# Kernel tuning notes

Hardware: AMD Instinct MI355X
Metric: run time of the kernel (lower is better)

Reference implementation:

```python
import jax, jax.numpy as jnp
import numpy as np

H, D = 8, 16          # heads, head_dim
HID = H * D           # hidden_channels = 128
OUT = 64              # out_channels
N = 25_000            # nodes per node type (author, paper)
E = 250_000           # edges per relation
L = 2                 # num HGT layers
T = 2                 # node types
R = 2                 # edge types: (author->paper), (paper->author)
SCALE = 1.0 / np.sqrt(HID).astype(np.float32)


def setup_inputs() -> dict:
    key = jax.random.key(0)
    ks = jax.random.split(key, 16)
    f = lambda k, s: jax.random.normal(k, s, dtype=jnp.float32)
    return dict(
        x_author=f(ks[0], (N, HID)),
        x_paper=f(ks[1], (N, HID)),
        edge_writes=jax.random.randint(ks[2], (2, E), 0, N, dtype=jnp.int32),
        edge_rev=jax.random.randint(ks[3], (2, E), 0, N, dtype=jnp.int32),
        W_in=f(ks[4], (T, HID, HID)) * SCALE,
        b_in=jnp.zeros((T, HID), jnp.float32),
        Wq=f(ks[5], (L, T, HID, HID)) * SCALE,
        bq=jnp.zeros((L, T, HID), jnp.float32),
        Wk=f(ks[6], (L, T, HID, HID)) * SCALE,
        bk=jnp.zeros((L, T, HID), jnp.float32),
        Wv=f(ks[7], (L, T, HID, HID)) * SCALE,
        bv=jnp.zeros((L, T, HID), jnp.float32),
        Wa=f(ks[8], (L, T, HID, HID)) * SCALE,
        ba=jnp.zeros((L, T, HID), jnp.float32),
        skip=jnp.ones((L, T), jnp.float32),
        a_rel=f(ks[9], (L, R, H, D, D)) * (1.0 / np.sqrt(D).astype(np.float32)),
        m_rel=f(ks[10], (L, R, H, D, D)) * (1.0 / np.sqrt(D).astype(np.float32)),
        p_rel=jnp.ones((L, R, H), jnp.float32),
        W_out=f(ks[11], (HID, OUT)) * SCALE,
        b_out=jnp.zeros((OUT,), jnp.float32),
    )


def _seg_softmax(scores, seg, n):
    # scores [E, H]; softmax over edges sharing the same destination node.
    m = jax.ops.segment_max(scores, seg, num_segments=n)
    e = jnp.exp(scores - m[seg])
    s = jax.ops.segment_sum(e, seg, num_segments=n)
    return e / (s[seg] + 1e-16)


def _hnn_forward(x_author, x_paper, edge_writes, edge_rev, W_in, b_in, Wq, bq,
                 Wk, bk, Wv, bv, Wa, ba, skip, a_rel, m_rel, p_rel, W_out, b_out):
    # input projection per node type + relu
    xs = [jax.nn.relu(x_author @ W_in[0] + b_in[0]),
          jax.nn.relu(x_paper @ W_in[1] + b_in[1])]
    edges = [(0, 1, edge_writes), (1, 0, edge_rev)]  # (src_type, dst_type, edge_index)
    inv_sqrt_d = jnp.float32(1.0 / np.sqrt(D))
    for l in range(L):
        q = [(xs[t] @ Wq[l, t] + bq[l, t]).reshape(N, H, D) for t in range(T)]
        k = [(xs[t] @ Wk[l, t] + bk[l, t]).reshape(N, H, D) for t in range(T)]
        v = [(xs[t] @ Wv[l, t] + bv[l, t]).reshape(N, H, D) for t in range(T)]
        agg = [jnp.zeros((N, HID), xs[0].dtype) for _ in range(T)]
        for r, (s, t, ei) in enumerate(edges):
            src, dst = ei[0], ei[1]
            # per-relation transform of gathered keys/values: [E,H,D] x [H,D,D]
            k_e = jnp.einsum('ehd,hdf->ehf', k[s][src], a_rel[l, r])
            score = jnp.sum(q[t][dst] * k_e, axis=-1) * p_rel[l, r] * inv_sqrt_d  # [E,H]
            alpha = _seg_softmax(score, dst, N)
            v_e = jnp.einsum('ehd,hdf->ehf', v[s][src], m_rel[l, r])
            msg = (v_e * alpha[:, :, None]).reshape(E, HID)
            agg[t] = agg[t] + jax.ops.segment_sum(msg, dst, num_segments=N)
        new_xs = []
        for t in range(T):
            out = jax.nn.gelu(agg[t], approximate=False) @ Wa[l, t] + ba[l, t]
            beta = jax.nn.sigmoid(skip[l, t])
            new_xs.append(beta * out + (1.0 - beta) * xs[t])  # gated residual (in==out dims)
        xs = new_xs
    return (xs[0] @ W_out + b_out, xs[1] @ W_out + b_out)


def reference(x_author, x_paper, edge_writes, edge_rev, W_in, b_in, Wq, bq, Wk,
              bk, Wv, bv, Wa, ba, skip, a_rel, m_rel, p_rel, W_out, b_out):
    return _hnn_forward(x_author, x_paper, edge_writes, edge_rev, W_in, b_in,
                        Wq, bq, Wk, bk, Wv, bv, Wa, ba, skip, a_rel, m_rel,
                        p_rel, W_out, b_out)
```

## Files before the change

### kernel.cpp

```cpp
#include <hip/hip_runtime.h>
#include <math.h>

#define N_NODES 25000
#define E_EDGES 250000
#define HID 128
#define OUTC 64
#define NPB 98

using bf16x8 = __attribute__((ext_vector_type(8))) short;
using u16x8  = __attribute__((ext_vector_type(8))) unsigned short;
using f32x4  = __attribute__((ext_vector_type(4))) float;

__device__ __forceinline__ unsigned short f2bf(float f) {
    unsigned u = __float_as_uint(f);
    u = (u + 0x7fffu + ((u >> 16) & 1u)) >> 16;
    return (unsigned short)u;
}
__device__ __forceinline__ float bf2f(unsigned short h) {
    return __uint_as_float(((unsigned)h) << 16);
}
__device__ __forceinline__ float gelu_f(float x) {
    return 0.5f * x * (1.0f + erff(x * 0.70710678118654752440f));
}

__global__ void hist2(const int* __restrict__ e0, const int* __restrict__ e1,
                      int* __restrict__ cnt) {
    int r = blockIdx.y;
    const int* d = (r ? e1 : e0) + E_EDGES;
    int e = blockIdx.x * 256 + threadIdx.x;
    if (e < E_EDGES) atomicAdd(&cnt[r * N_NODES + d[e]], 1);
}

__global__ void csr_partial(const int* __restrict__ cnt, int* __restrict__ part) {
    int r = blockIdx.y, b = blockIdx.x, t = threadIdx.x;
    int idx = b * 256 + t;
    int v = (idx < N_NODES) ? cnt[r * N_NODES + idx] : 0;
    #pragma unroll
    for (int d = 1; d < 64; d <<= 1) v += __shfl_xor(v, d);
    __shared__ int ws[4];
    if ((t & 63) == 0) ws[t >> 6] = v;
    __syncthreads();
    if (t == 0) part[r * NPB + b] = ws[0] + ws[1] + ws[2] + ws[3];
}

__global__ void csr_scanpart(int* __restrict__ part) {
    int w = threadIdx.x >> 6, lane = threadIdx.x & 63;
    int base = w * NPB;
    int a = part[base + lane];
    int b = (lane < NPB - 64) ? part[base + 64 + lane] : 0;
    int va = a, vb = b;
    #pragma unroll
    for (int d = 1; d < 64; d <<= 1) { int u = __shfl_up(va, d); if (lane >= d) va += u; }
    #pragma unroll
    for (int d = 1; d < 64; d <<= 1) { int u = __shfl_up(vb, d); if (lane >= d) vb += u; }
    int tot0 = __shfl(va, 63);
    part[base + lane] = va - a;
    if (lane < NPB - 64) part[base + 64 + lane] = vb - b + tot0;
}

__global__ void csr_write(int* __restrict__ cnt, const int* __restrict__ part,
                          int* __restrict__ rowptr) {
    int r = blockIdx.y, b = blockIdx.x, t = threadIdx.x;
    int idx = b * 256 + t;
    int v = (idx < N_NODES) ? cnt[r * N_NODES + idx] : 0;
    int lane = t & 63, w = t >> 6;
    int iv = v;
    #pragma unroll
    for (int d = 1; d < 64; d <<= 1) { int u = __shfl_up(iv, d); if (lane >= d) iv += u; }
    __shared__ int wtot[4];
    if (lane == 63) wtot[w] = iv;
    __syncthreads();
    int woff = part[r * NPB + b];
    #pragma unroll
    for (int i = 0; i < 4; i++) if (i < w) woff += wtot[i];
    int excl = woff + iv - v;
    if (idx < N_NODES) {
        rowptr[r * (N_NODES + 1) + idx] = excl;
        cnt[r * N_NODES + idx] = excl;
    }
    if (b == 0 && t == 0) rowptr[r * (N_NODES + 1) + N_NODES] = E_EDGES;
}

__global__ void scatter2(const int* __restrict__ e0, const int* __restrict__ e1,
                         int* __restrict__ cursor, int* __restrict__ srcs) {
    int r = blockIdx.y;
    const int* e = r ? e1 : e0;
    int i = blockIdx.x * 256 + threadIdx.x;
    if (i < E_EDGES) {
        int p = atomicAdd(&cursor[r * N_NODES + e[E_EDGES + i]], 1);
        srcs[r * E_EDGES + p] = e[i];
    }
}

__global__ void tconv(const float* __restrict__ src, unsigned short* __restrict__ dst, int C) {
    int m = blockIdx.y;
    int idx = blockIdx.x * 256 + threadIdx.x;
    if (idx >= C * 128) return;
    int c = idx >> 7, k = idx & 127;
    dst[(size_t)m * C * 128 + idx] = f2bf(src[(size_t)m * 128 * C + k * C + c]);
}

__global__ __launch_bounds__(256) void prep_qkv(
    const float* __restrict__ Wq, const float* __restrict__ bq,
    const float* __restrict__ Wk, const float* __restrict__ bk,
    const float* __restrict__ Wv, const float* __restrict__ bv,
    const float* __restrict__ a_rel, const float* __restrict__ m_rel,
    unsigned short* __restrict__ WT, float* __restrict__ bfq)
{
    int p = blockIdx.y;
    __shared__ float sA[2048], sM[2048];
    for (int i = threadIdx.x; i < 2048; i += 256) {
        sA[i] = a_rel[p * 2048 + i];
        sM[i] = m_rel[p * 2048 + i];
    }
    __syncthreads();
    int idx = blockIdx.x * 256 + threadIdx.x;
    if (idx >= 384 * 129) return;
    int c = idx / 129;
    int ik = idx - c * 129;
    const float* wq = Wq + (size_t)p * 16384;
    const float* wk = Wk + (size_t)p * 16384;
    const float* wv = Wv + (size_t)p * 16384;
    float val;
    if (c < 128) {
        val = (ik < 128) ? wq[ik * 128 + c] : bq[p * 128 + c];
    } else if (c < 256) {
        int cc = c - 128, h = cc >> 4, f = cc & 15;
        const float* row = (ik < 128) ? &wk[ik * 128 + h * 16] : &bk[p * 128 + h * 16];
        float s = 0.f;
        #pragma unroll
        for (int d = 0; d < 16; d++) s = fmaf(row[d], sA[h * 256 + d * 16 + f], s);
        val = s;
    } else {
        int cc = c - 256, h = cc >> 4, f = cc & 15;
        const float* row = (ik < 128) ? &wv[ik * 128 + h * 16] : &bv[p * 128 + h * 16];
        float s = 0.f;
        #pragma unroll
        for (int d = 0; d < 16; d++) s = fmaf(row[d], sM[h * 256 + d * 16 + f], s);
        val = s;
    }
    if (ik < 128) WT[(size_t)p * 384 * 128 + (size_t)c * 128 + ik] = f2bf(val);
    else bfq[p * 384 + c] = val;
}

template<int NOUT, int BN, int OUTMODE, int A_FP32, int KVIL>
__global__ __launch_bounds__(256) void mm4_kernel(
    const void* __restrict__ A0, const void* __restrict__ A1,
    const unsigned short* __restrict__ W0, const unsigned short* __restrict__ W1,
    const float* __restrict__ b0, const float* __restrict__ b1,
    const unsigned short* __restrict__ res0, const unsigned short* __restrict__ res1,
    const float* __restrict__ skipp,
    void* __restrict__ C0, void* __restrict__ C1, int nrows)
{
    constexpr int CF = BN / 16;
    __shared__ unsigned short sW[BN * 128];
    int z = blockIdx.z;
    const void* Av = z ? A1 : A0;
    const unsigned short* W = z ? W1 : W0;
    const float* bias = z ? b1 : b0;
    const unsigned short* res = z ? res1 : res0;
    void* Cv = z ? C1 : C0;

    int t = threadIdx.x;
    int w = t >> 6, lane = t & 63, lo = lane & 15, hi = lane >> 4;
    int col0 = blockIdx.y * BN;
    int rowbase = blockIdx.x * 128 + w * 32;

    const unsigned short* Wg = W + (size_t)col0 * 128;
    #pragma unroll
    for (int it = 0; it < BN / 16; ++it) {
        int idx = it * 256 + t;
        int col = idx >> 4, ch = idx & 15;
        bf16x8 v = *(const bf16x8*)(Wg + (size_t)col * 128 + ch * 8);
        *(bf16x8*)&sW[col * 128 + ((ch ^ (col & 7)) << 3)] = v;
    }

    bf16x8 a[2][4];
    #pragma unroll
    for (int rf = 0; rf < 2; rf++) {
        int r = rowbase + rf * 16 + lo;
        if (r > nrows - 1) r = nrows - 1;
        if (A_FP32) {
            const float* Arow = (const float*)Av + (size_t)r * HID;
            #pragma unroll
            for (int kk = 0; kk < 4; kk++) {
                float4 x0 = *(const float4*)(Arow + kk * 32 + hi * 8);
                float4 x1 = *(const float4*)(Arow + kk * 32 + hi * 8 + 4);
                bf16x8 v;
                v[0] = (short)f2bf(x0.x); v[1] = (short)f2bf(x0.y);
                v[2] = (short)f2bf(x0.z); v[3] = (short)f2bf(x0.w);
                v[4] = (short)f2bf(x1.x); v[5] = (short)f2bf(x1.y);
                v[6] = (short)f2bf(x1.z); v[7] = (short)f2bf(x1.w);
                a[rf][kk] = v;
            }
        } else {
            const unsigned short* Arow = (const unsigned short*)Av + (size_t)r * HID;
            #pragma unroll
            for (int kk = 0; kk < 4; kk++)
                a[rf][kk] = *(const bf16x8*)(Arow + kk * 32 + hi * 8);
        }
    }
    __syncthreads();

    f32x4 acc[2][CF];
    #pragma unroll
    for (int rf = 0; rf < 2; rf++)
        #pragma unroll
        for (int cf = 0; cf < CF; cf++) acc[rf][cf] = (f32x4){0.f, 0.f, 0.f, 0.f};

    #pragma unroll
    for (int cf = 0; cf < CF; cf++) {
        int colb = cf * 16 + lo;
        int sbase = colb * 128;
        int sx = colb & 7;
        bf16x8 bfr[4];
        #pragma unroll
        for (int kk = 0; kk < 4; kk++) {
            int ch = kk * 4 + hi;
            bfr[kk] = *(const bf16x8*)&sW[sbase + ((ch ^ sx) << 3)];
        }
        #pragma unroll
        for (int kk = 0; kk < 4; kk++) {
            acc[0][cf] = __builtin_amdgcn_mfma_f32_16x16x32_bf16(a[0][kk], bfr[kk], acc[0][cf], 0, 0, 0);
            acc[1][cf] = __builtin_amdgcn_mfma_f32_16x16x32_bf16(a[1][kk], bfr[kk], acc[1][cf], 0, 0, 0);
        }
    }

    float beta = 0.f, omb = 0.f;
    if (OUTMODE == 2) { float sv = skipp[z]; beta = 1.f / (1.f + __expf(-sv)); omb = 1.f - beta; }
    #pragma unroll
    for (int rf = 0; rf < 2; rf++) {
        #pragma unroll
        for (int cf = 0; cf < CF; cf++) {
            int col = col0 + cf * 16 + lo;
            float bb = bias[col];
            int scol = col;
            if (KVIL) {
                if (col >= 256)      { int cc = col - 256; scol = 128 + ((cc >> 2) << 3) + 4 + (cc & 3); }
                else if (col >= 128) { int cc = col - 128; scol = 128 + ((cc >> 2) << 3) + (cc & 3); }
            }
            #pragma unroll
            for (int j = 0; j < 4; j++) {
                int r = rowbase + rf * 16 + hi * 4 + j;
                if (r >= nrows) continue;
                float v = acc[rf][cf][j] + bb;
                if (OUTMODE == 1) v = fmaxf(v, 0.f);
                if (OUTMODE == 2) v = beta * v + omb * bf2f(res[(size_t)r * NOUT + col]);
                if (OUTMODE == 3) ((float*)Cv)[(size_t)r * NOUT + col] = v;
                else ((unsigned short*)Cv)[(size_t)r * NOUT + scol] = f2bf(v);
            }
        }
    }
}

__global__ __launch_bounds__(256) void attn5_kernel(
    const unsigned short* __restrict__ qkv0, const unsigned short* __restrict__ qkv1,
    const int* __restrict__ rowptr, const int* __restrict__ srcs,
    const float* __restrict__ prel,
    unsigned short* __restrict__ agg0, unsigned short* __restrict__ agg1, int n)
{
    int r = blockIdx.y;
    const unsigned short* qd = r ? qkv0 : qkv1;
    const unsigned short* sv = r ? qkv1 : qkv0;
    unsigned short* agg      = r ? agg0 : agg1;
    const int* rp = rowptr + r * (N_NODES + 1);
    const int* ss = srcs + r * E_EDGES;

    int nid = blockIdx.x * 4 + (threadIdx.x >> 6);
    if (nid >= n) return;
    int lane = threadIdx.x & 63;
    int half = lane >> 5;
    int g = lane & 31;
    int c0 = g << 2;
    int h = g >> 2;
    int goff = 128 + (g << 3);

    const unsigned short* qrow = qd + (size_t)nid * 384 + c0;
    float q0 = bf2f(qrow[0]), q1 = bf2f(qrow[1]), q2 = bf2f(qrow[2]), q3 = bf2f(qrow[3]);
    float p = prel[r * 8 + h] * 0.25f;

    float mA = -1e30f, sA = 0.f, aA0 = 0.f, aA1 = 0.f, aA2 = 0.f, aA3 = 0.f;
    float mB = -1e30f, sB = 0.f, aB0 = 0.f, aB1 = 0.f, aB2 = 0.f, aB3 = 0.f;
    int beg = rp[nid], end = rp[nid + 1];
    int i0 = beg + half;
    if (i0 < end) {
        int e1 = end - 1;
        int cA = i0 < e1 ? i0 : e1;
        int cB = i0 + 2 < e1 ? i0 + 2 : e1;
        u16x8 kvA = *(const u16x8*)(sv + (size_t)ss[cA] * 384 + goff);
        u16x8 kvB = *(const u16x8*)(sv + (size_t)ss[cB] * 384 + goff);
        int nA = i0 + 4 < e1 ? i0 + 4 : e1;
        int nB = i0 + 6 < e1 ? i0 + 6 : e1;
        int idxAn = ss[nA];
        int idxBn = ss[nB];
        for (int i = i0; i < end; i += 4) {
            u16x8 kvAn = *(const u16x8*)(sv + (size_t)idxAn * 384 + goff);
            u16x8 kvBn = *(const u16x8*)(sv + (size_t)idxBn * 384 + goff);
            int pA = i + 8 < e1 ? i + 8 : e1;
            int pB = i + 10 < e1 ? i + 10 : e1;
            int idxAnn = ss[pA];
            int idxBnn = ss[pB];
            {
                float sc = q0 * bf2f(kvA[0]) + q1 * bf2f(kvA[1]) + q2 * bf2f(kvA[2]) + q3 * bf2f(kvA[3]);
                sc += __shfl_xor(sc, 1);
                sc += __shfl_xor(sc, 2);
                float score = sc * p;
                float nm = fmaxf(mA, score);
                float rsc = __expf(mA - nm);
                float e = __expf(score - nm);
                sA = sA * rsc + e;
                aA0 = aA0 * rsc + e * bf2f(kvA[4]);
                aA1 = aA1 * rsc + e * bf2f(kvA[5]);
                aA2 = aA2 * rsc + e * bf2f(kvA[6]);
                aA3 = aA3 * rsc + e * bf2f(kvA[7]);
                mA = nm;
            }
            if (i + 2 < end) {
                float sc = q0 * bf2f(kvB[0]) + q1 * bf2f(kvB[1]) + q2 * bf2f(kvB[2]) + q3 * bf2f(kvB[3]);
                sc += __shfl_xor(sc, 1);
                sc += __shfl_xor(sc, 2);
                float score = sc * p;
                float nm = fmaxf(mB, score);
                float rsc = __expf(mB - nm);
                float e = __expf(score - nm);
                sB = sB * rsc + e;
                aB0 = aB0 * rsc + e * bf2f(kvB[4]);
                aB1 = aB1 * rsc + e * bf2f(kvB[5]);
                aB2 = aB2 * rsc + e * bf2f(kvB[6]);
                aB3 = aB3 * rsc + e * bf2f(kvB[7]);
                mB = nm;
            }
            kvA = kvAn; kvB = kvBn; idxAn = idxAnn; idxBn = idxBnn;
        }
        float nm = fmaxf(mA, mB);
        float fA = __expf(mA - nm), fB = __expf(mB - nm);
        sA = sA * fA + sB * fB;
        aA0 = aA0 * fA + aB0 * fB;
        aA1 = aA1 * fA + aB1 * fB;
        aA2 = aA2 * fA + aB2 * fB;
        aA3 = aA3 * fA + aB3 * fB;
        mA = nm;
    }
    float mo = __shfl_xor(mA, 32);
    float nm2 = fmaxf(mA, mo);
    float f = __expf(mA - nm2);
    sA *= f; aA0 *= f; aA1 *= f; aA2 *= f; aA3 *= f;
    sA += __shfl_xor(sA, 32);
    aA0 += __shfl_xor(aA0, 32);
    aA1 += __shfl_xor(aA1, 32);
    aA2 += __shfl_xor(aA2, 32);
    aA3 += __shfl_xor(aA3, 32);

    if (half == 0) {
        float inv = 1.f / (sA + 1e-16f);
        ushort4 o;
        o.x = f2bf(gelu_f(aA0 * inv)); o.y = f2bf(gelu_f(aA1 * inv));
        o.z = f2bf(gelu_f(aA2 * inv)); o.w = f2bf(gelu_f(aA3 * inv));
        *(ushort4*)(agg + (size_t)nid * HID + c0) = o;
    }
}

extern "C" void kernel_launch(void* const* d_in, const int* in_sizes, int n_in,
                              void* d_out, int out_size, void* d_ws, size_t ws_size,
                              hipStream_t stream)
{
    (void)in_sizes; (void)n_in; (void)out_size; (void)ws_size;
    const float* x_author = (const float*)d_in[0];
    const float* x_paper  = (const float*)d_in[1];
    const int*   e_writes = (const int*)d_in[2];
    const int*   e_rev    = (const int*)d_in[3];
    const float* W_in = (const float*)d_in[4];
    const float* b_in = (const float*)d_in[5];
    const float* Wq = (const float*)d_in[6];
    const float* bq = (const float*)d_in[7];
    const float* Wk = (const float*)d_in[8];
    const float* bk = (const float*)d_in[9];
    const float* Wv = (const float*)d_in[10];
    const float* bv = (const float*)d_in[11];
    const float* Wa = (const float*)d_in[12];
    const float* ba = (const float*)d_in[13];
    const float* skip = (const float*)d_in[14];
    const float* a_rel = (const float*)d_in[15];
    const float* m_rel = (const float*)d_in[16];
    const float* p_rel = (const float*)d_in[17];
    const float* W_out = (const float*)d_in[18];
    const float* b_out = (const float*)d_in[19];
    float* out = (float*)d_out;

    const size_t NC = (size_t)N_NODES * HID;
    const size_t NQ = (size_t)N_NODES * 384;
    unsigned short* U = (unsigned short*)d_ws;
    unsigned short* cur0 = U;             unsigned short* cur1 = U + NC;
    unsigned short* agg0 = U + 2 * NC;    unsigned short* agg1 = U + 3 * NC;
    unsigned short* qkv0 = U + 4 * NC;    unsigned short* qkv1 = U + 4 * NC + NQ;
    unsigned short* WTin  = U + 4 * NC + 2 * NQ;
    unsigned short* WTqkv = WTin + 2 * 16384;
    unsigned short* WTa   = WTqkv + 4 * 49152;
    unsigned short* WTout = WTa + 4 * 16384;
    float* bfq = (float*)(WTout + OUTC * 128);
    int* I      = (int*)(bfq + 4 * 384);
    int* cnt    = I;
    int* part   = I + 2 * N_NODES;
    int* rowptr = part + 2 * NPB;
    int* srcs   = rowptr + 2 * (N_NODES + 1);

    dim3 blk(256);
    int eGrid = (E_EDGES + 255) / 256;
    int mmX = (N_NODES + 127) / 128;
    int attnX = (N_NODES + 3) / 4;
    int prepX = (384 * 129 + 255) / 256;

    hipMemsetAsync(cnt, 0, 2 * N_NODES * sizeof(int), stream);
    hist2<<<dim3(eGrid, 2), blk, 0, stream>>>(e_writes, e_rev, cnt);
    csr_partial<<<dim3(NPB, 2), blk, 0, stream>>>(cnt, part);
    csr_scanpart<<<1, 128, 0, stream>>>(part);
    csr_write<<<dim3(NPB, 2), blk, 0, stream>>>(cnt, part, rowptr);
    scatter2<<<dim3(eGrid, 2), blk, 0, stream>>>(e_writes, e_rev, cnt, srcs);

    tconv<<<dim3(64, 2), blk, 0, stream>>>(W_in, WTin, HID);
    tconv<<<dim3(64, 4), blk, 0, stream>>>(Wa, WTa, HID);
    tconv<<<dim3(32, 1), blk, 0, stream>>>(W_out, WTout, OUTC);
    prep_qkv<<<dim3(prepX, 4), blk, 0, stream>>>(Wq, bq, Wk, bk, Wv, bv, a_rel, m_rel, WTqkv, bfq);

    mm4_kernel<HID, 128, 1, 1, 0><<<dim3(mmX, 1, 2), blk, 0, stream>>>(
        x_author, x_paper, WTin, WTin + 16384, b_in, b_in + HID,
        nullptr, nullptr, nullptr, cur0, cur1, N_NODES);

    for (int l = 0; l < 2; l++) {
        mm4_kernel<384, 128, 0, 0, 1><<<dim3(mmX, 3, 2), blk, 0, stream>>>(
            cur0, cur1,
            WTqkv + (size_t)(l * 2 + 0) * 49152, WTqkv + (size_t)(l * 2 + 1) * 49152,
            bfq + (l * 2 + 0) * 384, bfq + (l * 2 + 1) * 384,
            nullptr, nullptr, nullptr, qkv0, qkv1, N_NODES);
        attn5_kernel<<<dim3(attnX, 2), blk, 0, stream>>>(
            qkv0, qkv1, rowptr, srcs, p_rel + (size_t)l * 16, agg0, agg1, N_NODES);
        mm4_kernel<HID, 128, 2, 0, 0><<<dim3(mmX, 1, 2), blk, 0, stream>>>(
            agg0, agg1,
            WTa + (size_t)(l * 2 + 0) * 16384, WTa + (size_t)(l * 2 + 1) * 16384,
            ba + (l * 2 + 0) * HID, ba + (l * 2 + 1) * HID,
            cur0, cur1, skip + l * 2, cur0, cur1, N_NODES);
    }

    mm4_kernel<OUTC, 64, 3, 0, 0><<<dim3(mmX, 1, 2), blk, 0, stream>>>(
        cur0, cur1, WTout, WTout, b_out, b_out,
        nullptr, nullptr, nullptr, out, out + (size_t)N_NODES * OUTC, N_NODES);
}
```

Baseline: 372.1 us.

## Use lazy-rescale exp2 online softmax and fold K/V interleave into weights

The attention online softmax now works in base 2 with the log2e factor folded into the score scale. It rescales the running max only when a new score exceeds it by more than a threshold, which removes one exponential and several multiplies per edge in the common case. The K/V column interleaving moves from the QKV GEMM epilogue into the weight-prep kernel, and the three weight-transpose launches are merged into one. The lazy rescale lets accumulators grow by up to 2^8 before renormalising, which slightly changes numerics and overflow headroom.

```diff
diff --git a/kernel.cpp b/kernel.cpp
--- a/kernel.cpp
+++ b/kernel.cpp
@@ -21,6 +21,9 @@
 }
 __device__ __forceinline__ float gelu_f(float x) {
     return 0.5f * x * (1.0f + erff(x * 0.70710678118654752440f));
+}
+__device__ __forceinline__ float ex2(float x) {
+    return __builtin_amdgcn_exp2f(x);
 }
 
 __global__ void hist2(const int* __restrict__ e0, const int* __restrict__ e1,
@@ -92,12 +95,25 @@
     }
 }
 
-__global__ void tconv(const float* __restrict__ src, unsigned short* __restrict__ dst, int C) {
-    int m = blockIdx.y;
+__global__ void tconv_all(const float* __restrict__ W_in, const float* __restrict__ Wa,
+                          const float* __restrict__ W_out,
+                          unsigned short* __restrict__ WTin, unsigned short* __restrict__ WTa,
+                          unsigned short* __restrict__ WTout) {
     int idx = blockIdx.x * 256 + threadIdx.x;
-    if (idx >= C * 128) return;
-    int c = idx >> 7, k = idx & 127;
-    dst[(size_t)m * C * 128 + idx] = f2bf(src[(size_t)m * 128 * C + k * C + c]);
+    if (idx < 32768) {
+        int m = idx >> 14, rr = idx & 16383;
+        int c = rr >> 7, k = rr & 127;
+        WTin[idx] = f2bf(W_in[m * 16384 + k * 128 + c]);
+    } else if (idx < 32768 + 65536) {
+        int j = idx - 32768;
+        int m = j >> 14, rr = j & 16383;
+        int c = rr >> 7, k = rr & 127;
+        WTa[j] = f2bf(Wa[m * 16384 + k * 128 + c]);
+    } else if (idx < 32768 + 65536 + 8192) {
+        int j = idx - 98304;
+        int c = j >> 7, k = j & 127;
+        WTout[j] = f2bf(W_out[k * 64 + c]);
+    }
 }
 
 __global__ __launch_bounds__(256) void prep_qkv(
@@ -124,26 +140,30 @@
     float val;
     if (c < 128) {
         val = (ik < 128) ? wq[ik * 128 + c] : bq[p * 128 + c];
-    } else if (c < 256) {
-        int cc = c - 128, h = cc >> 4, f = cc & 15;
-        const float* row = (ik < 128) ? &wk[ik * 128 + h * 16] : &bk[p * 128 + h * 16];
+    } else {
+        int u = c - 128;
+        int gg = u >> 3, w = u & 7;
+        int cc = (gg << 2) + (w & 3);
+        int h = cc >> 4, f = cc & 15;
+        const float* row;
+        const float* tab;
+        if (w < 4) {
+            row = (ik < 128) ? &wk[ik * 128 + h * 16] : &bk[p * 128 + h * 16];
+            tab = &sA[h * 256];
+        } else {
+            row = (ik < 128) ? &wv[ik * 128 + h * 16] : &bv[p * 128 + h * 16];
+            tab = &sM[h * 256];
+        }
         float s = 0.f;
         #pragma unroll
-        for (int d = 0; d < 16; d++) s = fmaf(row[d], sA[h * 256 + d * 16 + f], s);
-        val = s;
-    } else {
-        int cc = c - 256, h = cc >> 4, f = cc & 15;
-        const float* row = (ik < 128) ? &wv[ik * 128 + h * 16] : &bv[p * 128 + h * 16];
-        float s = 0.f;
-        #pragma unroll
-        for (int d = 0; d < 16; d++) s = fmaf(row[d], sM[h * 256 + d * 16 + f], s);
+        for (int d = 0; d < 16; d++) s = fmaf(row[d], tab[d * 16 + f], s);
         val = s;
     }
     if (ik < 128) WT[(size_t)p * 384 * 128 + (size_t)c * 128 + ik] = f2bf(val);
     else bfq[p * 384 + c] = val;
 }
 
-template<int NOUT, int BN, int OUTMODE, int A_FP32, int KVIL>
+template<int NOUT, int BN, int OUTMODE, int A_FP32>
 __global__ __launch_bounds__(256) void mm4_kernel(
     const void* __restrict__ A0, const void* __restrict__ A1,
     const unsigned short* __restrict__ W0, const unsigned short* __restrict__ W1,
@@ -234,11 +254,6 @@
         for (int cf = 0; cf < CF; cf++) {
             int col = col0 + cf * 16 + lo;
             float bb = bias[col];
-            int scol = col;
-            if (KVIL) {
-                if (col >= 256)      { int cc = col - 256; scol = 128 + ((cc >> 2) << 3) + 4 + (cc & 3); }
-                else if (col >= 128) { int cc = col - 128; scol = 128 + ((cc >> 2) << 3) + (cc & 3); }
-            }
             #pragma unroll
             for (int j = 0; j < 4; j++) {
                 int r = rowbase + rf * 16 + hi * 4 + j;
@@ -247,13 +262,13 @@
                 if (OUTMODE == 1) v = fmaxf(v, 0.f);
                 if (OUTMODE == 2) v = beta * v + omb * bf2f(res[(size_t)r * NOUT + col]);
                 if (OUTMODE == 3) ((float*)Cv)[(size_t)r * NOUT + col] = v;
-                else ((unsigned short*)Cv)[(size_t)r * NOUT + scol] = f2bf(v);
+                else ((unsigned short*)Cv)[(size_t)r * NOUT + col] = f2bf(v);
             }
         }
     }
 }
 
-__global__ __launch_bounds__(256) void attn5_kernel(
+__global__ __launch_bounds__(256) void attn6_kernel(
     const unsigned short* __restrict__ qkv0, const unsigned short* __restrict__ qkv1,
     const int* __restrict__ rowptr, const int* __restrict__ srcs,
     const float* __restrict__ prel,
@@ -277,7 +292,7 @@
 
     const unsigned short* qrow = qd + (size_t)nid * 384 + c0;
     float q0 = bf2f(qrow[0]), q1 = bf2f(qrow[1]), q2 = bf2f(qrow[2]), q3 = bf2f(qrow[3]);
-    float p = prel[r * 8 + h] * 0.25f;
+    float p2 = prel[r * 8 + h] * 0.25f * 1.44269504088896f;
 
     float mA = -1e30f, sA = 0.f, aA0 = 0.f, aA1 = 0.f, aA2 = 0.f, aA3 = 0.f;
     float mB = -1e30f, sB = 0.f, aB0 = 0.f, aB1 = 0.f, aB2 = 0.f, aB3 = 0.f;
@@ -304,36 +319,40 @@
                 float sc = q0 * bf2f(kvA[0]) + q1 * bf2f(kvA[1]) + q2 * bf2f(kvA[2]) + q3 * bf2f(kvA[3]);
                 sc += __shfl_xor(sc, 1);
                 sc += __shfl_xor(sc, 2);
-                float score = sc * p;
-                float nm = fmaxf(mA, score);
-                float rsc = __expf(mA - nm);
-                float e = __expf(score - nm);
-                sA = sA * rsc + e;
-                aA0 = aA0 * rsc + e * bf2f(kvA[4]);
-                aA1 = aA1 * rsc + e * bf2f(kvA[5]);
-                aA2 = aA2 * rsc + e * bf2f(kvA[6]);
-                aA3 = aA3 * rsc + e * bf2f(kvA[7]);
-                mA = nm;
+                float sc2 = sc * p2;
+                if (sc2 > mA + 8.f) {
+                    float rsc = ex2(mA - sc2);
+                    sA *= rsc; aA0 *= rsc; aA1 *= rsc; aA2 *= rsc; aA3 *= rsc;
+                    mA = sc2;
+                }
+                float e = ex2(sc2 - mA);
+                sA += e;
+                aA0 = fmaf(e, bf2f(kvA[4]), aA0);
+                aA1 = fmaf(e, bf2f(kvA[5]), aA1);
+                aA2 = fmaf(e, bf2f(kvA[6]), aA2);
+                aA3 = fmaf(e, bf2f(kvA[7]), aA3);
             }
             if (i + 2 < end) {
                 float sc = q0 * bf2f(kvB[0]) + q1 * bf2f(kvB[1]) + q2 * bf2f(kvB[2]) + q3 * bf2f(kvB[3]);
                 sc += __shfl_xor(sc, 1);
                 sc += __shfl_xor(sc, 2);
-                float score = sc * p;
-                float nm = fmaxf(mB, score);
-                float rsc = __expf(mB - nm);
-                float e = __expf(score - nm);
-                sB = sB * rsc + e;
-                aB0 = aB0 * rsc + e * bf2f(kvB[4]);
-                aB1 = aB1 * rsc + e * bf2f(kvB[5]);
-                aB2 = aB2 * rsc + e * bf2f(kvB[6]);
-                aB3 = aB3 * rsc + e * bf2f(kvB[7]);
-                mB = nm;
+                float sc2 = sc * p2;
+                if (sc2 > mB + 8.f) {
+                    float rsc = ex2(mB - sc2);
+                    sB *= rsc; aB0 *= rsc; aB1 *= rsc; aB2 *= rsc; aB3 *= rsc;
+                    mB = sc2;
+                }
+                float e = ex2(sc2 - mB);
+                sB += e;
+                aB0 = fmaf(e, bf2f(kvB[4]), aB0);
+                aB1 = fmaf(e, bf2f(kvB[5]), aB1);
+                aB2 = fmaf(e, bf2f(kvB[6]), aB2);
+                aB3 = fmaf(e, bf2f(kvB[7]), aB3);
             }
             kvA = kvAn; kvB = kvBn; idxAn = idxAnn; idxBn = idxBnn;
         }
         float nm = fmaxf(mA, mB);
-        float fA = __expf(mA - nm), fB = __expf(mB - nm);
+        float fA = ex2(mA - nm), fB = ex2(mB - nm);
         sA = sA * fA + sB * fB;
         aA0 = aA0 * fA + aB0 * fB;
         aA1 = aA1 * fA + aB1 * fB;
@@ -343,7 +362,7 @@
     }
     float mo = __shfl_xor(mA, 32);
     float nm2 = fmaxf(mA, mo);
-    float f = __expf(mA - nm2);
+    float f = ex2(mA - nm2);
     sA *= f; aA0 *= f; aA1 *= f; aA2 *= f; aA3 *= f;
     sA += __shfl_xor(sA, 32);
     aA0 += __shfl_xor(aA0, 32);
@@ -409,39 +428,38 @@
     int mmX = (N_NODES + 127) / 128;
     int attnX = (N_NODES + 3) / 4;
     int prepX = (384 * 129 + 255) / 256;
-
-    hipMemsetAsync(cnt, 0, 2 * N_NODES * sizeof(int), stream);
+    int tcX = (32768 + 65536 + 8192 + 255) / 256;
+
+    (void)hipMemsetAsync(cnt, 0, 2 * N_NODES * sizeof(int), stream);
     hist2<<<dim3(eGrid, 2), blk, 0, stream>>>(e_writes, e_rev, cnt);
     csr_partial<<<dim3(NPB, 2), blk, 0, stream>>>(cnt, part);
     csr_scanpart<<<1, 128, 0, stream>>>(part);
     csr_write<<<dim3(NPB, 2), blk, 0, stream>>>(cnt, part, rowptr);
     scatter2<<<dim3(eGrid, 2), blk, 0, stream>>>(e_writes, e_rev, cnt, srcs);
 
-    tconv<<<dim3(64, 2), blk, 0, stream>>>(W_in, WTin, HID);
-    tconv<<<dim3(64, 4), blk, 0, stream>>>(Wa, WTa, HID);
-    tconv<<<dim3(32, 1), blk, 0, stream>>>(W_out, WTout, OUTC);
+    tconv_all<<<tcX, blk, 0, stream>>>(W_in, Wa, W_out, WTin, WTa, WTout);
     prep_qkv<<<dim3(prepX, 4), blk, 0, stream>>>(Wq, bq, Wk, bk, Wv, bv, a_rel, m_rel, WTqkv, bfq);
 
-    mm4_kernel<HID, 128, 1, 1, 0><<<dim3(mmX, 1, 2), blk, 0, stream>>>(
+    mm4_kernel<HID, 128, 1, 1><<<dim3(mmX, 1, 2), blk, 0, stream>>>(
         x_author, x_paper, WTin, WTin + 16384, b_in, b_in + HID,
         nullptr, nullptr, nullptr, cur0, cur1, N_NODES);
 
     for (int l = 0; l < 2; l++) {
-        mm4_kernel<384, 128, 0, 0, 1><<<dim3(mmX, 3, 2), blk, 0, stream>>>(
+        mm4_kernel<384, 128, 0, 0><<<dim3(mmX, 3, 2), blk, 0, stream>>>(
             cur0, cur1,
             WTqkv + (size_t)(l * 2 + 0) * 49152, WTqkv + (size_t)(l * 2 + 1) * 49152,
             bfq + (l * 2 + 0) * 384, bfq + (l * 2 + 1) * 384,
             nullptr, nullptr, nullptr, qkv0, qkv1, N_NODES);
-        attn5_kernel<<<dim3(attnX, 2), blk, 0, stream>>>(
+        attn6_kernel<<<dim3(attnX, 2), blk, 0, stream>>>(
             qkv0, qkv1, rowptr, srcs, p_rel + (size_t)l * 16, agg0, agg1, N_NODES);
-        mm4_kernel<HID, 128, 2, 0, 0><<<dim3(mmX, 1, 2), blk, 0, stream>>>(
+        mm4_kernel<HID, 128, 2, 0><<<dim3(mmX, 1, 2), blk, 0, stream>>>(
             agg0, agg1,
             WTa + (size_t)(l * 2 + 0) * 16384, WTa + (size_t)(l * 2 + 1) * 16384,
             ba + (l * 2 + 0) * HID, ba + (l * 2 + 1) * HID,
             cur0, cur1, skip + l * 2, cur0, cur1, N_NODES);
     }
 
-    mm4_kernel<OUTC, 64, 3, 0, 0><<<dim3(mmX, 1, 2), blk, 0, stream>>>(
+    mm4_kernel<OUTC, 64, 3, 0><<<dim3(mmX, 1, 2), blk, 0, stream>>>(
         cur0, cur1, WTout, WTout, b_out, b_out,
         nullptr, nullptr, nullptr, out, out + (size_t)N_NODES * OUTC, N_NODES);
 }
```

Measured after the change: 360.2 us. 1.03x faster.
